# Performance work log

Measured on AMD Instinct MI355X. Metric: run time of the kernel, lower is better.

The kernel has to match this reference:

```python
import jax, jax.numpy as jnp
import numpy as np

B, S = 32, 256          # sequences, tokens per sequence (prefill)
DIM, NH, NKV, HD = 2048, 16, 16, 128
CLS, GRID, BASE = 1, 16, 10000


def precompute_freqs_cis_2d(grid_size, n_elem, base, cls_token_num):
    half = n_elem // 2
    freqs = 1.0 / (base ** (np.arange(0, half, 2)[: half // 2].astype(np.float32) / half))
    t = np.arange(grid_size, dtype=np.float32)
    fr = np.outer(t, freqs)                      # [grid, half//2]
    fg = np.concatenate([
        np.broadcast_to(fr[:, None, :], (grid_size, grid_size, fr.shape[1])),
        np.broadcast_to(fr[None, :, :], (grid_size, grid_size, fr.shape[1])),
    ], axis=-1)                                  # [grid, grid, half]
    cache = np.stack([np.cos(fg), np.sin(fg)], axis=-1).reshape(grid_size * grid_size, half, 2)
    cond = np.concatenate([np.zeros((cls_token_num, half, 2), np.float32), cache.astype(np.float32)], axis=0)
    return jnp.asarray(cond)                     # [cls+grid^2, half, 2]

FREQS = precompute_freqs_cis_2d(GRID, HD, BASE, CLS)


def _apply_rope(x, fc):
    # x: [T, H, HD], fc: [T, HD//2, 2]
    xr = x.reshape(x.shape[0], x.shape[1], HD // 2, 2)
    c = fc[:, None, :, 0]
    s = fc[:, None, :, 1]
    out = jnp.stack([xr[..., 0] * c - xr[..., 1] * s,
                     xr[..., 1] * c + xr[..., 0] * s], axis=-1)
    return out.reshape(x.shape)


def setup_inputs() -> dict:
    key = jax.random.key(0)
    k1, k2, k3 = jax.random.split(key, 3)
    x = jax.random.normal(k1, (B * S, DIM), dtype=jnp.float32)
    positions = jnp.tile(jnp.arange(S, dtype=jnp.int32), B)  # per-seq positions 0..S-1
    total_kv = (NH + 2 * NKV) * HD
    wqkv = jax.random.normal(k2, (total_kv, DIM), dtype=jnp.float32) * 0.02
    wo = jax.random.normal(k3, (DIM, DIM), dtype=jnp.float32) * 0.02
    return {"x": x, "positions": positions, "wqkv": wqkv, "wo": wo}


def reference(x, positions, wqkv, wo):
    T = x.shape[0]
    kv_size = NKV * HD
    qkv = x @ wqkv.T                               # [T, dim + 2*kv_size]
    xq, xk, xv = jnp.split(qkv, [DIM, DIM + kv_size], axis=-1)
    q = xq.reshape(T, NH, HD)
    k = xk.reshape(T, NKV, HD)
    v = xv.reshape(T, NKV, HD)

    fc = FREQS[positions]                          # [T, HD//2, 2]
    q = _apply_rope(q, fc)
    k = _apply_rope(k, fc)

    # paged attention (prefill): causal attention within each sequence
    qb = q.reshape(B, S, NH, HD)
    kb = k.reshape(B, S, NKV, HD)
    vb = v.reshape(B, S, NKV, HD)
    scale = HD ** -0.5
    scores = jnp.einsum("bqhd,bkhd->bhqk", qb, kb) * scale   # [B,H,S,S]
    causal = jnp.tril(jnp.ones((S, S), dtype=bool))
    scores = jnp.where(causal[None, None], scores, jnp.finfo(scores.dtype).min)
    attn = jax.nn.softmax(scores, axis=-1)
    out = jnp.einsum("bhqk,bkhd->bqhd", attn, vb).reshape(T, DIM)
    return out @ wo.T
```

## Files before the change

### kernel.cpp

```cpp
#include <hip/hip_runtime.h>
#include <cstddef>


typedef float    f32x4 __attribute__((ext_vector_type(4)));
typedef _Float16 f16x8 __attribute__((ext_vector_type(8)));
typedef _Float16 f16x4 __attribute__((ext_vector_type(4)));

#define LOG2E 1.4426950408889634f
#define NLOG2B_32 (-0.41524101186192697f)

__device__ static inline f32x4 mfma16x32(f16x8 a, f16x8 b, f32x4 c) {
  return __builtin_amdgcn_mfma_f32_16x16x32_f16(a, b, c, 0, 0, 0);
}

__device__ static inline void gload16(const void* g, void* lds) {
  __builtin_amdgcn_global_load_lds(
      (const __attribute__((address_space(1))) unsigned int*)g,
      (__attribute__((address_space(3))) unsigned int*)lds, 16, 0, 0);
}

#define BAR()    asm volatile("s_barrier" ::: "memory")
#define VMCNT6() asm volatile("s_waitcnt vmcnt(6)" ::: "memory")

__global__ void cvt3_f32_f16(const float* __restrict__ s0, _Float16* __restrict__ d0,
                             const float* __restrict__ s1, _Float16* __restrict__ d1,
                             const float* __restrict__ s2, _Float16* __restrict__ d2) {
  int i = blockIdx.x * blockDim.x + threadIdx.x;
  const float* src; _Float16* dst;
  if (i < 4194304)      { src = s0; dst = d0; }
  else if (i < 7340032) { src = s1; dst = d1; i -= 4194304; }
  else                  { src = s2; dst = d2; i -= 7340032; }
  f32x4 v = *(const f32x4*)(src + (size_t)i * 4);
  f16x4 o;
  o[0] = (_Float16)v[0]; o[1] = (_Float16)v[1];
  o[2] = (_Float16)v[2]; o[3] = (_Float16)v[3];
  *(f16x4*)(dst + (size_t)i * 4) = o;
}

template <typename OutT>
__global__ void __launch_bounds__(512, 2)
gemm_bt5(const _Float16* __restrict__ A, const _Float16* __restrict__ Bt,
         OutT* __restrict__ C, int M, int N, int K) {
  __shared__ __attribute__((aligned(16))) _Float16 Ab[2][256 * 64];
  __shared__ __attribute__((aligned(16))) _Float16 Bb[2][256 * 64];

  const int tid  = threadIdx.x;
  const int lane = tid & 63;
  const int w    = tid >> 6;
  const int wm   = w >> 2, wn = w & 3;
  const int g    = lane >> 4, li = lane & 15;

  const int nwg = (int)gridDim.x;
  const int cpx = nwg >> 3;
  const int bid = (int)blockIdx.x;
  const int swz = (bid & 7) * cpx + (bid >> 3);
  const int nbn = N >> 8;
  const int bm  = (swz / nbn) << 8;
  const int bn  = (swz % nbn) << 8;
  const int NT  = K >> 6;

  const int srow = tid >> 3;
  const int scol = ((tid & 7) ^ (srow & 7)) * 8;
  const _Float16* gA = A  + (size_t)(bm + srow) * K + scol;
  const _Float16* gB = Bt + (size_t)(bn + srow) * K + scol;
  const int sdst = w * 1024;

  auto stage = [&](const _Float16* gbase, _Float16* lbase, int h, int kt) {
    const _Float16* gp = gbase + (size_t)h * 128 * K + kt;
    char* lp = (char*)lbase + h * 16384;
#pragma unroll
    for (int j = 0; j < 2; ++j)
      gload16(gp + (size_t)j * 64 * K, lp + j * 8192 + sdst);
  };

  auto rdfrag = [&](const _Float16* buf, int row, int k2) -> f16x8 {
    const int pc = ((k2 << 2) + g) ^ (li & 7);
    return *(const f16x8*)((const char*)buf + row * 128 + pc * 16);
  };

  f32x4 acc[8][4] = {};

  stage(gA, Ab[0], 0, 0);
  stage(gB, Bb[0], 0, 0);
  stage(gB, Bb[0], 1, 0);
  stage(gA, Ab[0], 1, 0);
  stage(gA, Ab[1], 0, (NT > 1) ? 64 : 0);
  VMCNT6();
  BAR();

  for (int T = 0; T < NT; ++T) {
    const int cb = T & 1, nb = cb ^ 1;
    const _Float16* Ac = Ab[cb];
    const _Float16* Bc = Bb[cb];
    const int ktN  = (T + 1 < NT) ? (T + 1) << 6 : 0;
    const int ktN2 = (T + 2 < NT) ? (T + 2) << 6 : 0;

    f16x8 af0[4][2], af1[4][2], bf0[2][2], bf1[2][2];

#pragma unroll
    for (int m = 0; m < 4; ++m)
#pragma unroll
      for (int k2 = 0; k2 < 2; ++k2)
        af0[m][k2] = rdfrag(Ac, wm * 128 + m * 16 + li, k2);
#pragma unroll
    for (int n = 0; n < 2; ++n)
#pragma unroll
      for (int k2 = 0; k2 < 2; ++k2)
        bf0[n][k2] = rdfrag(Bc, wn * 64 + n * 16 + li, k2);
    stage(gB, Bb[nb], 0, ktN);
    __builtin_amdgcn_s_setprio(1);
#pragma unroll
    for (int m = 0; m < 4; ++m)
#pragma unroll
      for (int n = 0; n < 2; ++n)
#pragma unroll
        for (int k2 = 0; k2 < 2; ++k2)
          acc[m][n] = mfma16x32(af0[m][k2], bf0[n][k2], acc[m][n]);
    __builtin_amdgcn_s_setprio(0);
    BAR();

#pragma unroll
    for (int n = 0; n < 2; ++n)
#pragma unroll
      for (int k2 = 0; k2 < 2; ++k2)
        bf1[n][k2] = rdfrag(Bc, wn * 64 + (n + 2) * 16 + li, k2);
    stage(gB, Bb[nb], 1, ktN);
    __builtin_amdgcn_s_setprio(1);
#pragma unroll
    for (int m = 0; m < 4; ++m)
#pragma unroll
      for (int n = 0; n < 2; ++n)
#pragma unroll
        for (int k2 = 0; k2 < 2; ++k2)
          acc[m][n + 2] = mfma16x32(af0[m][k2], bf1[n][k2], acc[m][n + 2]);
    __builtin_amdgcn_s_setprio(0);
    VMCNT6();
    BAR();

#pragma unroll
    for (int m = 0; m < 4; ++m)
#pragma unroll
      for (int k2 = 0; k2 < 2; ++k2)
        af1[m][k2] = rdfrag(Ac, wm * 128 + (m + 4) * 16 + li, k2);
    stage(gA, Ab[nb], 1, ktN);
    __builtin_amdgcn_s_setprio(1);
#pragma unroll
    for (int m = 0; m < 4; ++m)
#pragma unroll
      for (int n = 0; n < 2; ++n)
#pragma unroll
        for (int k2 = 0; k2 < 2; ++k2)
          acc[m + 4][n] = mfma16x32(af1[m][k2], bf0[n][k2], acc[m + 4][n]);
    __builtin_amdgcn_s_setprio(0);
    BAR();

    stage(gA, Ab[cb], 0, ktN2);
    __builtin_amdgcn_s_setprio(1);
#pragma unroll
    for (int m = 0; m < 4; ++m)
#pragma unroll
      for (int n = 0; n < 2; ++n)
#pragma unroll
        for (int k2 = 0; k2 < 2; ++k2)
          acc[m + 4][n + 2] = mfma16x32(af1[m][k2], bf1[n][k2], acc[m + 4][n + 2]);
    __builtin_amdgcn_s_setprio(0);
    VMCNT6();
    BAR();
  }

  asm volatile("s_waitcnt vmcnt(0)" ::: "memory");

#pragma unroll
  for (int m = 0; m < 8; ++m)
#pragma unroll
    for (int n = 0; n < 4; ++n)
#pragma unroll
      for (int r = 0; r < 4; ++r) {
        const int row = bm + wm * 128 + m * 16 + g * 4 + r;
        const int col = bn + wn * 64 + n * 16 + li;
        C[(size_t)row * N + col] = (OutT)acc[m][n][r];
      }
}

__global__ void __launch_bounds__(512)
attn_kernel(const _Float16* __restrict__ qkv, _Float16* __restrict__ O,
            const int* __restrict__ positions) {
  const int b  = blockIdx.x >> 4;
  const int h  = blockIdx.x & 15;
  const int tb = b << 8;
  const int tid = threadIdx.x;
  const int lane = tid & 63;
  const int w = tid >> 6;
  const int g = lane >> 4, li = lane & 15;

  __shared__ __attribute__((aligned(16))) _Float16 Ks[64 * 128];
  __shared__ __attribute__((aligned(16))) _Float16 Vt[64 * 128];
  __shared__ __attribute__((aligned(16))) _Float16 Ps[8][32 * 40];
  __shared__ float2 tab[512];
  __shared__ int    ptab[256];

  {
    const float ang = (float)(tid >> 5) * exp2f((float)(tid & 31) * NLOG2B_32);
    float s, c;
    sincosf(ang, &s, &c);
    tab[tid] = make_float2(c, s);
    if (tid < 256) ptab[tid] = positions[tb + tid];
  }
  __syncthreads();

  const int qb[2]   = {w, 15 - w};
  const int qrow[2] = {qb[0] * 16, qb[1] * 16};
  const int kmax[2] = {qb[0] >> 2, qb[1] >> 2};

  const int jj = li >> 2;
  const int cc = li & 3;
  const unsigned vbase =
      (unsigned)(unsigned long long)(__attribute__((address_space(3))) _Float16*)Vt;

  f16x8 qf[2][4];
#pragma unroll
  for (int rb = 0; rb < 2; ++rb) {
    const int pos = ptab[qrow[rb] + li];
    const int iv = (pos - 1) >> 4, jv = (pos - 1) & 15;
#pragma unroll
    for (int ks = 0; ks < 4; ++ks) {
      f16x8 v = *(const f16x8*)(qkv + (size_t)(tb + qrow[rb] + li) * 6144
                                + h * 128 + ks * 32 + g * 8);
      f16x8 o;
      if (pos == 0) {
#pragma unroll
        for (int u = 0; u < 8; ++u) o[u] = (_Float16)0.f;
      } else {
        const int tv = (ks < 2) ? iv : jv;
#pragma unroll
        for (int u = 0; u < 4; ++u) {
          const float2 cs = tab[tv * 32 + ((ks * 16 + g * 4 + u) & 31)];
          const float x0 = (float)v[2 * u], x1 = (float)v[2 * u + 1];
          o[2 * u]     = (_Float16)(x0 * cs.x - x1 * cs.y);
          o[2 * u + 1] = (_Float16)(x1 * cs.x + x0 * cs.y);
        }
      }
      qf[rb][ks] = o;
    }
  }

  f32x4 oacc[2][8] = {};
  float m_r[2][4], l_r[2][4];
#pragma unroll
  for (int rb = 0; rb < 2; ++rb)
#pragma unroll
    for (int r = 0; r < 4; ++r) { m_r[rb][r] = -1e30f; l_r[rb][r] = 0.f; }

  const float scale = 0.08838834764831845f;

  for (int kt = 0; kt < 4; ++kt) {
#pragma unroll
    for (int i = 0; i < 2; ++i) {
      const int s = i * 512 + tid;
      const int key = s >> 4;
      const int sch = (s & 15) ^ (key & 7);
      const _Float16* gv = qkv + (size_t)(tb + kt * 64 + key) * 6144
                           + 4096 + h * 128 + sch * 8;
      gload16(gv, (char*)Vt + (i * 512 + (tid & ~63)) * 16);
    }
#pragma unroll
    for (int i = 0; i < 2; ++i) {
      const int s = i * 512 + tid;
      const int key = s >> 4;
      const int c   = s & 15;
      f16x8 v = *(const f16x8*)(qkv + (size_t)(tb + kt * 64 + key) * 6144
                                + 2048 + h * 128 + c * 8);
      const int pos = ptab[kt * 64 + key];
      f16x8 o;
      if (pos == 0) {
#pragma unroll
        for (int u = 0; u < 8; ++u) o[u] = (_Float16)0.f;
      } else {
        const int iv = (pos - 1) >> 4, jv = (pos - 1) & 15;
        const int tv = (c < 8) ? iv : jv;
#pragma unroll
        for (int u = 0; u < 4; ++u) {
          const float2 cs = tab[tv * 32 + ((c * 4 + u) & 31)];
          const float x0 = (float)v[2 * u], x1 = (float)v[2 * u + 1];
          o[2 * u]     = (_Float16)(x0 * cs.x - x1 * cs.y);
          o[2 * u + 1] = (_Float16)(x1 * cs.x + x0 * cs.y);
        }
      }
      *(f16x8*)((char*)Ks + key * 256 + (c ^ (key & 7)) * 16) = o;
    }
    __syncthreads();

    const bool act[2] = {kt <= kmax[0], kt <= kmax[1]};
    if (act[0] || act[1]) {
      f32x4 sacc[2][4] = {};
#pragma unroll
      for (int ks = 0; ks < 4; ++ks) {
        f16x8 kf[4];
#pragma unroll
        for (int cb = 0; cb < 4; ++cb) {
          const int key = cb * 16 + li;
          const int chunk = (ks * 4 + g) ^ (key & 7);
          kf[cb] = *(const f16x8*)((const char*)Ks + key * 256 + chunk * 16);
        }
#pragma unroll
        for (int rb = 0; rb < 2; ++rb)
          if (act[rb])
#pragma unroll
            for (int cb = 0; cb < 4; ++cb)
              sacc[rb][cb] = mfma16x32(qf[rb][ks], kf[cb], sacc[rb][cb]);
      }
#pragma unroll
      for (int rb = 0; rb < 2; ++rb) {
        if (!act[rb]) continue;
#pragma unroll
        for (int r = 0; r < 4; ++r) {
          const int q = qrow[rb] + g * 4 + r;
          float mx = -1e30f;
#pragma unroll
          for (int cb = 0; cb < 4; ++cb) {
            float sv = sacc[rb][cb][r] * scale;
            const int key = kt * 64 + cb * 16 + li;
            sv = (key <= q) ? sv : -1e30f;
            sacc[rb][cb][r] = sv;
            mx = fmaxf(mx, sv);
          }
#pragma unroll
          for (int off = 1; off < 16; off <<= 1)
            mx = fmaxf(mx, __shfl_xor(mx, off));
          const float mold = m_r[rb][r];
          const float mnew = fmaxf(mold, mx);
          const float alpha = exp2f((mold - mnew) * LOG2E);
          float rsum = 0.f;
#pragma unroll
          for (int cb = 0; cb < 4; ++cb) {
            const float pv = exp2f((sacc[rb][cb][r] - mnew) * LOG2E);
            sacc[rb][cb][r] = pv;
            rsum += pv;
          }
#pragma unroll
          for (int off = 1; off < 16; off <<= 1)
            rsum += __shfl_xor(rsum, off);
          m_r[rb][r] = mnew;
          l_r[rb][r] = l_r[rb][r] * alpha + rsum;
#pragma unroll
          for (int db = 0; db < 8; ++db)
            oacc[rb][db][r] *= alpha;
        }
      }
#pragma unroll
      for (int ks2 = 0; ks2 < 2; ++ks2) {
#pragma unroll
        for (int rb = 0; rb < 2; ++rb) {
          if (!act[rb]) continue;
#pragma unroll
          for (int cbh = 0; cbh < 2; ++cbh) {
            const int cb = ks2 * 2 + cbh;
#pragma unroll
            for (int r = 0; r < 4; ++r)
              Ps[w][(rb * 16 + g * 4 + r) * 40 + cbh * 16 + li] =
                  (_Float16)sacc[rb][cb][r];
          }
        }
        asm volatile("s_waitcnt lgkmcnt(0)" ::: "memory");
        f16x8 pa[2];
#pragma unroll
        for (int rb = 0; rb < 2; ++rb)
          if (act[rb])
            pa[rb] = *(const f16x8*)(&Ps[w][(rb * 16 + li) * 40 + g * 8]);

        f16x4 vlo[8], vhi[8];
        const int rowA = ks2 * 32 + g * 8 + jj;
        const unsigned base1 = vbase + (unsigned)(rowA * 256 + (cc & 1) * 8);
        const unsigned base2 = base1 + 4 * 256;
#pragma unroll
        for (int db = 0; db < 8; ++db) {
          const int ch = db * 2 + (cc >> 1);
          const unsigned a1 = base1 + (unsigned)((ch ^ jj) << 4);
          const unsigned a2 = base2 + (unsigned)((ch ^ jj ^ 4) << 4);
          asm volatile("ds_read_b64_tr_b16 %0, %1" : "=v"(vlo[db]) : "v"(a1));
          asm volatile("ds_read_b64_tr_b16 %0, %1" : "=v"(vhi[db]) : "v"(a2));
        }
        asm volatile("s_waitcnt lgkmcnt(0)" ::: "memory");
        __builtin_amdgcn_sched_barrier(0);
#pragma unroll
        for (int db = 0; db < 8; ++db) {
          const f16x8 vf = __builtin_shufflevector(vlo[db], vhi[db],
                                                   0, 1, 2, 3, 4, 5, 6, 7);
#pragma unroll
          for (int rb = 0; rb < 2; ++rb)
            if (act[rb])
              oacc[rb][db] = mfma16x32(pa[rb], vf, oacc[rb][db]);
        }
      }
    }
    __syncthreads();
  }
#pragma unroll
  for (int rb = 0; rb < 2; ++rb)
#pragma unroll
    for (int db = 0; db < 8; ++db)
#pragma unroll
      for (int r = 0; r < 4; ++r) {
        const int row = tb + qrow[rb] + g * 4 + r;
        const int col = h * 128 + db * 16 + li;
        O[(size_t)row * 2048 + col] = (_Float16)(oacc[rb][db][r] / l_r[rb][r]);
      }
}

extern "C" void kernel_launch(void* const* d_in, const int* in_sizes, int n_in,
                              void* d_out, int out_size, void* d_ws, size_t ws_size,
                              hipStream_t stream) {
  const float* x         = (const float*)d_in[0];
  const int*   positions = (const int*)d_in[1];
  const float* wqkv      = (const float*)d_in[2];
  const float* wo        = (const float*)d_in[3];
  float* out = (float*)d_out;

  char* ws = (char*)d_ws;
  _Float16* qkv    = (_Float16*)(ws);
  _Float16* xf     = (_Float16*)(ws + 100663296);
  _Float16* wqkvf  = (_Float16*)(ws + 134217728);
  _Float16* wof    = (_Float16*)(ws + 159383552);
  _Float16* of     = xf;

  cvt3_f32_f16<<<32768, 256, 0, stream>>>(x, xf, wqkv, wqkvf, wo, wof);

  gemm_bt5<_Float16><<<768, 512, 0, stream>>>(xf, wqkvf, qkv, 8192, 6144, 2048);

  attn_kernel<<<512, 512, 0, stream>>>(qkv, of, positions);

  gemm_bt5<float><<<256, 512, 0, stream>>>(of, wof, out, 8192, 2048, 2048);
}
```

Measured before the change: 346.0 us.

## Double-buffer V tiles and prefetch K into registers across attention key tiles

Makes the V shared-memory tile double-buffered and issues the next tile's async V load and K register load before computing the current tile. This overlaps global-memory latency with the QK/PV MFMA work. RoPE on the prefetched K is applied after a barrier, once the current tile's compute is done. Shared memory use grows by one V tile (16KB), which could reduce occupancy. The explicit waitcnt/barrier sequencing also needs care, since a missing wait could race.

```diff
diff --git a/kernel.cpp b/kernel.cpp
--- a/kernel.cpp
+++ b/kernel.cpp
@@ -194,11 +194,61 @@
   const int g = lane >> 4, li = lane & 15;
 
   __shared__ __attribute__((aligned(16))) _Float16 Ks[64 * 128];
-  __shared__ __attribute__((aligned(16))) _Float16 Vt[64 * 128];
+  __shared__ __attribute__((aligned(16))) _Float16 Vt[2][64 * 128];
   __shared__ __attribute__((aligned(16))) _Float16 Ps[8][32 * 40];
   __shared__ float2 tab[512];
   __shared__ int    ptab[256];
 
+  auto issueV = [&](int kt, int vb) {
+#pragma unroll
+    for (int i = 0; i < 2; ++i) {
+      const int s = i * 512 + tid;
+      const int key = s >> 4;
+      const int sch = (s & 15) ^ (key & 7);
+      gload16(qkv + (size_t)(tb + kt * 64 + key) * 6144 + 4096 + h * 128 + sch * 8,
+              (char*)Vt[vb] + (i * 512 + (tid & ~63)) * 16);
+    }
+  };
+
+  f16x8 kreg[2];
+  auto loadK = [&](int kt) {
+#pragma unroll
+    for (int i = 0; i < 2; ++i) {
+      const int s = i * 512 + tid;
+      const int key = s >> 4;
+      const int c = s & 15;
+      kreg[i] = *(const f16x8*)(qkv + (size_t)(tb + kt * 64 + key) * 6144
+                                + 2048 + h * 128 + c * 8);
+    }
+  };
+  auto ropeWriteK = [&](int kt) {
+#pragma unroll
+    for (int i = 0; i < 2; ++i) {
+      const int s = i * 512 + tid;
+      const int key = s >> 4;
+      const int c = s & 15;
+      const int pos = ptab[kt * 64 + key];
+      const f16x8 v = kreg[i];
+      f16x8 o;
+      if (pos == 0) {
+#pragma unroll
+        for (int u = 0; u < 8; ++u) o[u] = (_Float16)0.f;
+      } else {
+        const int iv = (pos - 1) >> 4, jv = (pos - 1) & 15;
+        const int tv = (c < 8) ? iv : jv;
+#pragma unroll
+        for (int u = 0; u < 4; ++u) {
+          const float2 cs = tab[tv * 32 + ((c * 4 + u) & 31)];
+          const float x0 = (float)v[2 * u], x1 = (float)v[2 * u + 1];
+          o[2 * u]     = (_Float16)(x0 * cs.x - x1 * cs.y);
+          o[2 * u + 1] = (_Float16)(x1 * cs.x + x0 * cs.y);
+        }
+      }
+      *(f16x8*)((char*)Ks + key * 256 + (c ^ (key & 7)) * 16) = o;
+    }
+  };
+
+  issueV(0, 0);
   {
     const float ang = (float)(tid >> 5) * exp2f((float)(tid & 31) * NLOG2B_32);
     float s, c;
@@ -206,7 +256,8 @@
     tab[tid] = make_float2(c, s);
     if (tid < 256) ptab[tid] = positions[tb + tid];
   }
-  __syncthreads();
+  asm volatile("s_waitcnt lgkmcnt(0)" ::: "memory");
+  BAR();
 
   const int qb[2]   = {w, 15 - w};
   const int qrow[2] = {qb[0] * 16, qb[1] * 16};
@@ -244,6 +295,11 @@
     }
   }
 
+  loadK(0);
+  ropeWriteK(0);
+  asm volatile("s_waitcnt vmcnt(0) lgkmcnt(0)" ::: "memory");
+  BAR();
+
   f32x4 oacc[2][8] = {};
   float m_r[2][4], l_r[2][4];
 #pragma unroll
@@ -254,41 +310,11 @@
   const float scale = 0.08838834764831845f;
 
   for (int kt = 0; kt < 4; ++kt) {
-#pragma unroll
-    for (int i = 0; i < 2; ++i) {
-      const int s = i * 512 + tid;
-      const int key = s >> 4;
-      const int sch = (s & 15) ^ (key & 7);
-      const _Float16* gv = qkv + (size_t)(tb + kt * 64 + key) * 6144
-                           + 4096 + h * 128 + sch * 8;
-      gload16(gv, (char*)Vt + (i * 512 + (tid & ~63)) * 16);
-    }
-#pragma unroll
-    for (int i = 0; i < 2; ++i) {
-      const int s = i * 512 + tid;
-      const int key = s >> 4;
-      const int c   = s & 15;
-      f16x8 v = *(const f16x8*)(qkv + (size_t)(tb + kt * 64 + key) * 6144
-                                + 2048 + h * 128 + c * 8);
-      const int pos = ptab[kt * 64 + key];
-      f16x8 o;
-      if (pos == 0) {
-#pragma unroll
-        for (int u = 0; u < 8; ++u) o[u] = (_Float16)0.f;
-      } else {
-        const int iv = (pos - 1) >> 4, jv = (pos - 1) & 15;
-        const int tv = (c < 8) ? iv : jv;
-#pragma unroll
-        for (int u = 0; u < 4; ++u) {
-          const float2 cs = tab[tv * 32 + ((c * 4 + u) & 31)];
-          const float x0 = (float)v[2 * u], x1 = (float)v[2 * u + 1];
-          o[2 * u]     = (_Float16)(x0 * cs.x - x1 * cs.y);
-          o[2 * u + 1] = (_Float16)(x1 * cs.x + x0 * cs.y);
-        }
-      }
-      *(f16x8*)((char*)Ks + key * 256 + (c ^ (key & 7)) * 16) = o;
-    }
-    __syncthreads();
+    const int vb = kt & 1;
+    if (kt < 3) {
+      issueV(kt + 1, vb ^ 1);
+      loadK(kt + 1);
+    }
 
     const bool act[2] = {kt <= kmax[0], kt <= kmax[1]};
     if (act[0] || act[1]) {
@@ -370,7 +396,8 @@
 
         f16x4 vlo[8], vhi[8];
         const int rowA = ks2 * 32 + g * 8 + jj;
-        const unsigned base1 = vbase + (unsigned)(rowA * 256 + (cc & 1) * 8);
+        const unsigned base1 = vbase + (unsigned)(vb * 16384)
+                             + (unsigned)(rowA * 256 + (cc & 1) * 8);
         const unsigned base2 = base1 + 4 * 256;
 #pragma unroll
         for (int db = 0; db < 8; ++db) {
@@ -393,8 +420,13 @@
         }
       }
     }
-    __syncthreads();
+
+    BAR();
+    if (kt < 3) ropeWriteK(kt + 1);
+    asm volatile("s_waitcnt vmcnt(0) lgkmcnt(0)" ::: "memory");
+    BAR();
   }
+
 #pragma unroll
   for (int rb = 0; rb < 2; ++rb)
 #pragma unroll
```

Result: no change. 342.9 us (-0.9%).
